# Performance work log

Hardware: AMD Instinct MI355X
Metric: run time of the kernel (lower is better)

## Reference

```python
import jax, jax.numpy as jnp
import numpy as np

TAU_MIN = 0.1
TAU_MAX = 5.0
EPS = 1e-8


def setup_inputs() -> dict:
    key = jax.random.key(0)
    ks = jax.random.split(key, 5)
    B, DK, NK, DV, H = 16384, 512, 4096, 512, 32
    return {
        "q": jax.random.normal(ks[0], (B, DK), dtype=jnp.float32),
        "keys": jax.random.normal(ks[1], (NK, DK), dtype=jnp.float32),
        "values": jax.random.normal(ks[2], (NK, DV), dtype=jnp.float32),
        "w1": jax.random.normal(ks[3], (H, 1), dtype=jnp.float32) * (6.0 / (H + 1)) ** 0.5,
        "b1": jnp.zeros((H,), dtype=jnp.float32),
        "w2": jax.random.normal(ks[4], (1, H), dtype=jnp.float32) * (6.0 / (H + 1)) ** 0.5,
        "b2": jnp.zeros((1,), dtype=jnp.float32),
    }


def reference(q, keys, values, w1, b1, w2, b2):
    d_k = q.shape[-1]
    n_keys = keys.shape[0]
    base_scale = d_k ** -0.5
    max_entropy = np.log(max(n_keys, 2)).astype(np.float32)

    # raw logits: (B, NK)
    raw_logits = jnp.matmul(q, keys.T)

    # entropy of base-scaled softmax
    p = jax.nn.softmax(raw_logits * base_scale, axis=-1)
    entropy = -jnp.sum(p * jnp.log(p + EPS), axis=-1, keepdims=True)  # (B,1)
    entropy = jnp.clip(entropy / (max_entropy + EPS), 0.0, 1.0)

    # entropy -> tau via tiny MLP (exact GELU, matching torch default)
    h = jax.nn.gelu(entropy @ w1.T + b1, approximate=False)  # (B,H)
    scale = jax.nn.sigmoid(h @ w2.T + b2)                    # (B,1)
    tau = TAU_MIN + (TAU_MAX - TAU_MIN) * scale

    # re-scaled softmax and final matmul
    scaled_logits = raw_logits * base_scale / (tau + EPS)
    attn_weights = jax.nn.softmax(scaled_logits, axis=-1)    # (B, NK)
    output = jnp.matmul(attn_weights, values)                # (B, DV)
    return output, attn_weights, entropy, tau
```

## Files before the change

### kernel.cpp

```cpp
#include <hip/hip_runtime.h>
#include <math.h>

#define B_ROWS 16384
#define DK     512
#define NK     4096
#define DV     512
#define H_MLP  32

typedef __attribute__((ext_vector_type(8))) short s16x8;
typedef __attribute__((ext_vector_type(4))) short s16x4;
typedef __attribute__((ext_vector_type(4))) float f32x4;

__device__ __forceinline__ short f2bf(float f) {
  unsigned u = __float_as_uint(f);
  u += 0x7fffu + ((u >> 16) & 1u);
  return (short)(u >> 16);
}

__device__ __forceinline__ void async_cp16(const short* g, short* l) {
  __builtin_amdgcn_global_load_lds(
      (const __attribute__((address_space(1))) unsigned int*)g,
      (__attribute__((address_space(3))) unsigned int*)l, 16, 0, 0);
}

__global__ __launch_bounds__(256) void cvt_bf16(const float* __restrict__ src,
                                                short* __restrict__ dst,
                                                long n, float scale) {
  long i = ((long)blockIdx.x * 256 + threadIdx.x) * 8;
  if (i >= n) return;
  float4 a = *(const float4*)(src + i);
  float4 b = *(const float4*)(src + i + 4);
  s16x8 o;
  o[0] = f2bf(a.x * scale); o[1] = f2bf(a.y * scale);
  o[2] = f2bf(a.z * scale); o[3] = f2bf(a.w * scale);
  o[4] = f2bf(b.x * scale); o[5] = f2bf(b.y * scale);
  o[6] = f2bf(b.z * scale); o[7] = f2bf(b.w * scale);
  *(s16x8*)(dst + i) = o;
}

__global__ __launch_bounds__(256) void transpose_v(const float* __restrict__ v,
                                                   short* __restrict__ vT) {
  __shared__ float tile[32][33];
  const int tx = threadIdx.x & 31;
  const int ty = threadIdx.x >> 5;
  const int k0 = blockIdx.x * 32;
  const int n0 = blockIdx.y * 32;
#pragma unroll
  for (int j = 0; j < 4; ++j)
    tile[ty + j * 8][tx] = v[(long)(k0 + ty + j * 8) * DV + n0 + tx];
  __syncthreads();
#pragma unroll
  for (int j = 0; j < 4; ++j)
    vT[(long)(n0 + ty + j * 8) * NK + k0 + tx] = f2bf(tile[tx][ty + j * 8]);
}

__device__ __forceinline__ void stage_f32_sw(const float* __restrict__ src, int ldk,
                                             int row0, int k0, short* lds, int tid) {
#pragma unroll
  for (int i = 0; i < 4; ++i) {
    int f   = i * 256 + tid;
    int row = f >> 3;
    int p   = f & 7;
    int c   = p ^ (row & 7);
    const float* gp = src + (long)(row0 + row) * ldk + k0 + c * 8;
    float4 a = *(const float4*)gp;
    float4 b = *(const float4*)(gp + 4);
    s16x8 o;
    o[0] = f2bf(a.x); o[1] = f2bf(a.y); o[2] = f2bf(a.z); o[3] = f2bf(a.w);
    o[4] = f2bf(b.x); o[5] = f2bf(b.y); o[6] = f2bf(b.z); o[7] = f2bf(b.w);
    *(s16x8*)(lds + row * 64 + p * 8) = o;
  }
}

template <int RPW>
__device__ __forceinline__ void stage_bf_async(const short* __restrict__ src, int ldk,
                                               int row0, int k0, short* lds,
                                               int w, int lane) {
  const int srow = lane >> 3;
  const int c    = (lane & 7) ^ srow;
  const short* g = src + (long)(row0 + w * RPW + srow) * ldk + k0 + c * 8;
  short* lb = lds + w * RPW * 64;
#pragma unroll
  for (int i = 0; i < RPW / 8; ++i)
    async_cp16(g + (long)(i * 8) * ldk, lb + i * 512);
}

template <int AMODE, int BMODE>
__global__ __launch_bounds__(256) void gemm_nt(const void* __restrict__ Av,
                                               const void* __restrict__ Bv,
                                               float* __restrict__ C,
                                               int M, int N, int K, float alpha) {
  __shared__ short As[128 * 64];
  __shared__ short Bs[128 * 64];
  const int tid = threadIdx.x;

  const int nwg = gridDim.x * gridDim.y;
  const int bid = blockIdx.y * gridDim.x + blockIdx.x;
  const int per = nwg >> 3;
  const int swz = (bid & 7) * per + (bid >> 3);
  const int bx  = swz % gridDim.x;
  const int by  = swz / gridDim.x;

  const int rowBase = by * 128;
  const int colBase = bx * 128;
  const int w = tid >> 6, lane = tid & 63;
  const int waveM = w >> 1, waveN = w & 1;
  const int quad = lane >> 4, lr = lane & 15;
  const int sw = lr & 7;

  f32x4 acc[4][4];
#pragma unroll
  for (int i = 0; i < 4; ++i)
#pragma unroll
    for (int j = 0; j < 4; ++j)
      acc[i][j] = (f32x4){0.f, 0.f, 0.f, 0.f};

  for (int k0 = 0; k0 < K; k0 += 64) {
    __syncthreads();
    if constexpr (AMODE)
      stage_bf_async<32>((const short*)Av, K, rowBase, k0, As, w, lane);
    else
      stage_f32_sw((const float*)Av, K, rowBase, k0, As, tid);
    if constexpr (BMODE)
      stage_bf_async<32>((const short*)Bv, K, colBase, k0, Bs, w, lane);
    else
      stage_f32_sw((const float*)Bv, K, colBase, k0, Bs, tid);
    __syncthreads();
#pragma unroll
    for (int ks = 0; ks < 2; ++ks) {
      const int cpos = ((ks * 4 + quad) ^ sw) * 8;
      s16x8 a[4], b[4];
#pragma unroll
      for (int t = 0; t < 4; ++t) {
        a[t] = *(const s16x8*)(As + (waveM * 64 + t * 16 + lr) * 64 + cpos);
        b[t] = *(const s16x8*)(Bs + (waveN * 64 + t * 16 + lr) * 64 + cpos);
      }
#pragma unroll
      for (int mt = 0; mt < 4; ++mt)
#pragma unroll
        for (int nt = 0; nt < 4; ++nt)
          acc[mt][nt] = __builtin_amdgcn_mfma_f32_16x16x32_bf16(a[mt], b[nt], acc[mt][nt], 0, 0, 0);
    }
  }

#pragma unroll
  for (int mt = 0; mt < 4; ++mt)
#pragma unroll
    for (int nt = 0; nt < 4; ++nt) {
      int col = colBase + waveN * 64 + nt * 16 + lr;
#pragma unroll
      for (int r = 0; r < 4; ++r) {
        int row = rowBase + waveM * 64 + mt * 16 + quad * 4 + r;
        C[(long)row * N + col] = acc[mt][nt][r] * alpha;
      }
    }
}

template <int BM, int BN, int WM, int WN>
__global__ __launch_bounds__(WM * WN * 64, 2) void gemm_nt_2ph(
    const short* __restrict__ A, const short* __restrict__ B,
    float* __restrict__ C, int M, int N, int K, float alpha) {
  constexpr int NWAVE = WM * WN;
  constexpr int MR = BM / WM / 16;
  constexpr int NR = BN / WN / 16;
  __shared__ short As[2 * BM * 64];
  __shared__ short Bs[2 * BN * 64];

  const int tid = threadIdx.x;
  const int nwg = gridDim.x * gridDim.y;
  const int bid = blockIdx.y * gridDim.x + blockIdx.x;
  const int per = nwg >> 3;
  const int swz = (bid & 7) * per + (bid >> 3);
  const int bx  = swz % gridDim.x;
  const int by  = swz / gridDim.x;

  const int rowBase = by * BM;
  const int colBase = bx * BN;
  const int w = tid >> 6, lane = tid & 63;
  const int waveM = w / WN, waveN = w % WN;
  const int quad = lane >> 4, lr = lane & 15, sw = lr & 7;

  f32x4 acc[MR][NR];
#pragma unroll
  for (int i = 0; i < MR; ++i)
#pragma unroll
    for (int j = 0; j < NR; ++j)
      acc[i][j] = (f32x4){0.f, 0.f, 0.f, 0.f};

  auto compute = [&](const short* Ab, const short* Bb) {
#pragma unroll
    for (int ks = 0; ks < 2; ++ks) {
      const int cpos = ((ks * 4 + quad) ^ sw) * 8;
      s16x8 a[MR], b[NR];
#pragma unroll
      for (int mt = 0; mt < MR; ++mt)
        a[mt] = *(const s16x8*)(Ab + (waveM * (BM / WM) + mt * 16 + lr) * 64 + cpos);
#pragma unroll
      for (int nt = 0; nt < NR; ++nt)
        b[nt] = *(const s16x8*)(Bb + (waveN * (BN / WN) + nt * 16 + lr) * 64 + cpos);
      __builtin_amdgcn_s_setprio(1);
#pragma unroll
      for (int mt = 0; mt < MR; ++mt)
#pragma unroll
        for (int nt = 0; nt < NR; ++nt)
          acc[mt][nt] = __builtin_amdgcn_mfma_f32_16x16x32_bf16(a[mt], b[nt], acc[mt][nt], 0, 0, 0);
      __builtin_amdgcn_s_setprio(0);
    }
  };

  const int NT = K >> 6;

  stage_bf_async<BM / NWAVE>(A, K, rowBase, 0, As, w, lane);
  stage_bf_async<BN / NWAVE>(B, K, colBase, 0, Bs, w, lane);
  asm volatile("s_waitcnt vmcnt(0)" ::: "memory");
  __builtin_amdgcn_s_barrier();
  __builtin_amdgcn_sched_barrier(0);

  int cur = 0;
  for (int t = 0; t < NT - 1; ++t) {
    const int nxt = cur ^ 1;
    stage_bf_async<BM / NWAVE>(A, K, rowBase, (t + 1) * 64, As + nxt * BM * 64, w, lane);
    stage_bf_async<BN / NWAVE>(B, K, colBase, (t + 1) * 64, Bs + nxt * BN * 64, w, lane);
    __builtin_amdgcn_sched_barrier(0);
    compute(As + cur * BM * 64, Bs + cur * BN * 64);
    asm volatile("s_waitcnt vmcnt(0)" ::: "memory");
    __builtin_amdgcn_s_barrier();
    __builtin_amdgcn_sched_barrier(0);
    cur = nxt;
  }
  compute(As + cur * BM * 64, Bs + cur * BN * 64);

#pragma unroll
  for (int mt = 0; mt < MR; ++mt)
#pragma unroll
    for (int nt = 0; nt < NR; ++nt) {
      int col = colBase + waveN * (BN / WN) + nt * 16 + lr;
#pragma unroll
      for (int r = 0; r < 4; ++r) {
        int row = rowBase + waveM * (BM / WM) + mt * 16 + quad * 4 + r;
        C[(long)row * N + col] = acc[mt][nt][r] * alpha;
      }
    }
}

__global__ __launch_bounds__(256) void entropy_softmax(
    float* __restrict__ l, short* __restrict__ attn_bf,
    float* __restrict__ ent_out, float* __restrict__ tau_out,
    const float* __restrict__ w1, const float* __restrict__ b1,
    const float* __restrict__ w2, const float* __restrict__ b2) {
  const int wid = threadIdx.x >> 6, lane = threadIdx.x & 63;
  const int row = blockIdx.x * 4 + wid;
  float4* lr = (float4*)(l + (long)row * NK);

  float4 v[16];
#pragma unroll
  for (int it = 0; it < 16; ++it) v[it] = lr[it * 64 + lane];

  float m = -3.4e38f;
#pragma unroll
  for (int it = 0; it < 16; ++it)
    m = fmaxf(m, fmaxf(fmaxf(v[it].x, v[it].y), fmaxf(v[it].z, v[it].w)));
#pragma unroll
  for (int off = 32; off >= 1; off >>= 1) m = fmaxf(m, __shfl_xor(m, off));

  float Z = 0.f, E1 = 0.f;
#pragma unroll
  for (int it = 0; it < 16; ++it) {
    float e0 = __expf(v[it].x - m), e1 = __expf(v[it].y - m);
    float e2 = __expf(v[it].z - m), e3 = __expf(v[it].w - m);
    Z  += (e0 + e1) + (e2 + e3);
    E1 += v[it].x * e0 + v[it].y * e1 + v[it].z * e2 + v[it].w * e3;
  }
#pragma unroll
  for (int off = 32; off >= 1; off >>= 1) {
    Z  += __shfl_xor(Z, off);
    E1 += __shfl_xor(E1, off);
  }

  float entropy = m + __logf(Z) - E1 / Z;
  float en = fminf(fmaxf(entropy / 8.3177662f, 0.f), 1.f);

  float hp = 0.f;
  if (lane < H_MLP) {
    float x = en * w1[lane] + b1[lane];
    float g = 0.5f * x * (1.f + erff(x * 0.70710678f));
    hp = g * w2[lane];
  }
#pragma unroll
  for (int off = 16; off >= 1; off >>= 1) hp += __shfl_xor(hp, off);
  hp = __shfl(hp, 0);

  float s    = 1.f / (1.f + __expf(-(hp + b2[0])));
  float tau  = 0.1f + 4.9f * s;
  float itau = 1.f / (tau + 1e-8f);
  if (lane == 0) { ent_out[row] = en; tau_out[row] = tau; }

  const float mi = m * itau;
  float Z2 = 0.f;
#pragma unroll
  for (int it = 0; it < 16; ++it) {
    v[it].x = __expf(fmaf(v[it].x, itau, -mi));
    v[it].y = __expf(fmaf(v[it].y, itau, -mi));
    v[it].z = __expf(fmaf(v[it].z, itau, -mi));
    v[it].w = __expf(fmaf(v[it].w, itau, -mi));
    Z2 += (v[it].x + v[it].y) + (v[it].z + v[it].w);
  }
#pragma unroll
  for (int off = 32; off >= 1; off >>= 1) Z2 += __shfl_xor(Z2, off);
  const float inv = 1.f / Z2;

  short* br = attn_bf ? attn_bf + (long)row * NK : nullptr;
#pragma unroll
  for (int it = 0; it < 16; ++it) {
    float4 p;
    p.x = v[it].x * inv; p.y = v[it].y * inv;
    p.z = v[it].z * inv; p.w = v[it].w * inv;
    lr[it * 64 + lane] = p;
    if (br) {
      s16x4 o;
      o.x = f2bf(p.x); o.y = f2bf(p.y); o.z = f2bf(p.z); o.w = f2bf(p.w);
      *(s16x4*)(br + (it * 64 + lane) * 4) = o;
    }
  }
}

extern "C" void kernel_launch(void* const* d_in, const int* in_sizes, int n_in,
                              void* d_out, int out_size, void* d_ws, size_t ws_size,
                              hipStream_t stream) {
  const float* q    = (const float*)d_in[0];
  const float* keys = (const float*)d_in[1];
  const float* vals = (const float*)d_in[2];
  const float* w1   = (const float*)d_in[3];
  const float* b1   = (const float*)d_in[4];
  const float* w2   = (const float*)d_in[5];
  const float* b2   = (const float*)d_in[6];

  float* out  = (float*)d_out;
  float* attn = out + (long)B_ROWS * DV;
  float* ent  = attn + (long)B_ROWS * NK;
  float* tau  = ent + B_ROWS;

  char* ws = (char*)d_ws;
  const size_t off_vT    = 0;
  const size_t off_keysb = off_vT + (size_t)DV * NK * 2;
  const size_t off_qb    = off_keysb + (size_t)NK * DK * 2;
  const size_t off_attnb = off_qb + (size_t)B_ROWS * DK * 2;
  const size_t need_mid  = off_attnb;
  const size_t need_full = off_attnb + (size_t)B_ROWS * NK * 2;

  short* vT    = (short*)(ws + off_vT);
  short* keysb = (short*)(ws + off_keysb);
  short* qb    = (short*)(ws + off_qb);
  short* attnb = (short*)(ws + off_attnb);

  const float base_scale = 0.044194173824159216f;

  transpose_v<<<dim3(NK / 32, DV / 32), 256, 0, stream>>>(vals, vT);

  if (ws_size >= need_mid) {
    cvt_bf16<<<(int)(((long)B_ROWS * DK) / 2048), 256, 0, stream>>>(
        q, qb, (long)B_ROWS * DK, base_scale);
    cvt_bf16<<<(int)(((long)NK * DK) / 2048), 256, 0, stream>>>(
        keys, keysb, (long)NK * DK, 1.0f);
    gemm_nt_2ph<256, 256, 2, 4><<<dim3(NK / 256, B_ROWS / 256), 512, 0, stream>>>(
        qb, keysb, attn, B_ROWS, NK, DK, 1.0f);
  } else {
    gemm_nt<0, 0><<<dim3(NK / 128, B_ROWS / 128), 256, 0, stream>>>(
        q, keys, attn, B_ROWS, NK, DK, base_scale);
  }

  const bool full = ws_size >= need_full;
  entropy_softmax<<<B_ROWS / 4, 256, 0, stream>>>(
      attn, full ? attnb : nullptr, ent, tau, w1, b1, w2, b2);

  if (full)
    gemm_nt_2ph<128, 128, 2, 2><<<dim3(DV / 128, B_ROWS / 128), 256, 0, stream>>>(
        attnb, vT, out, B_ROWS, DV, NK, 1.0f);
  else
    gemm_nt<0, 1><<<dim3(DV / 128, B_ROWS / 128), 256, 0, stream>>>(
        attn, vT, out, B_ROWS, DV, NK, 1.0f);
}
```

Before: 609.3 us.

## Replace double-buffered GEMM with 4-stage K=32 async LDS pipeline

Measured after the change: 648.9 us. 1.06x slower.

```diff
diff --git a/kernel.cpp b/kernel.cpp
--- a/kernel.cpp
+++ b/kernel.cpp
@@ -156,15 +156,30 @@
     }
 }
 
+__device__ __forceinline__ void stage32(const short* __restrict__ src, int ldk,
+                                        int row0, int k0, short* lds,
+                                        int w, int lane) {
+  const int r16 = lane >> 2;
+  const int p   = lane & 3;
+  const int c   = p ^ ((r16 & 3) ^ (r16 >> 2));
+  const short* g = src + (long)(row0 + w * 32 + r16) * ldk + k0 + c * 8;
+  short* lb = lds + w * 32 * 32;
+  async_cp16(g, lb);
+  async_cp16(g + (long)16 * ldk, lb + 16 * 32);
+}
+
 template <int BM, int BN, int WM, int WN>
-__global__ __launch_bounds__(WM * WN * 64, 2) void gemm_nt_2ph(
+__global__ __launch_bounds__(WM * WN * 64, 2) void gemm_nt_p4(
     const short* __restrict__ A, const short* __restrict__ B,
     float* __restrict__ C, int M, int N, int K, float alpha) {
   constexpr int NWAVE = WM * WN;
   constexpr int MR = BM / WM / 16;
   constexpr int NR = BN / WN / 16;
-  __shared__ short As[2 * BM * 64];
-  __shared__ short Bs[2 * BN * 64];
+  constexpr int ASZ = BM * 32;
+  constexpr int BSZ = BN * 32;
+  static_assert(BM / NWAVE == 32 && BN / NWAVE == 32, "stage32 geometry");
+  __shared__ short As[4 * ASZ];
+  __shared__ short Bs[4 * BSZ];
 
   const int tid = threadIdx.x;
   const int nwg = gridDim.x * gridDim.y;
@@ -178,7 +193,9 @@
   const int colBase = bx * BN;
   const int w = tid >> 6, lane = tid & 63;
   const int waveM = w / WN, waveN = w % WN;
-  const int quad = lane >> 4, lr = lane & 15, sw = lr & 7;
+  const int quad = lane >> 4, lr = lane & 15;
+  const int sw2 = (lr & 3) ^ (lr >> 2);
+  const int cpos = (quad ^ sw2) * 8;
 
   f32x4 acc[MR][NR];
 #pragma unroll
@@ -188,47 +205,44 @@
       acc[i][j] = (f32x4){0.f, 0.f, 0.f, 0.f};
 
   auto compute = [&](const short* Ab, const short* Bb) {
-#pragma unroll
-    for (int ks = 0; ks < 2; ++ks) {
-      const int cpos = ((ks * 4 + quad) ^ sw) * 8;
-      s16x8 a[MR], b[NR];
-#pragma unroll
-      for (int mt = 0; mt < MR; ++mt)
-        a[mt] = *(const s16x8*)(Ab + (waveM * (BM / WM) + mt * 16 + lr) * 64 + cpos);
+    s16x8 a[MR], b[NR];
+#pragma unroll
+    for (int mt = 0; mt < MR; ++mt)
+      a[mt] = *(const s16x8*)(Ab + (waveM * (BM / WM) + mt * 16 + lr) * 32 + cpos);
+#pragma unroll
+    for (int nt = 0; nt < NR; ++nt)
+      b[nt] = *(const s16x8*)(Bb + (waveN * (BN / WN) + nt * 16 + lr) * 32 + cpos);
+    __builtin_amdgcn_s_setprio(1);
+#pragma unroll
+    for (int mt = 0; mt < MR; ++mt)
 #pragma unroll
       for (int nt = 0; nt < NR; ++nt)
-        b[nt] = *(const s16x8*)(Bb + (waveN * (BN / WN) + nt * 16 + lr) * 64 + cpos);
-      __builtin_amdgcn_s_setprio(1);
-#pragma unroll
-      for (int mt = 0; mt < MR; ++mt)
-#pragma unroll
-        for (int nt = 0; nt < NR; ++nt)
-          acc[mt][nt] = __builtin_amdgcn_mfma_f32_16x16x32_bf16(a[mt], b[nt], acc[mt][nt], 0, 0, 0);
-      __builtin_amdgcn_s_setprio(0);
-    }
+        acc[mt][nt] = __builtin_amdgcn_mfma_f32_16x16x32_bf16(a[mt], b[nt], acc[mt][nt], 0, 0, 0);
+    __builtin_amdgcn_s_setprio(0);
   };
 
-  const int NT = K >> 6;
-
-  stage_bf_async<BM / NWAVE>(A, K, rowBase, 0, As, w, lane);
-  stage_bf_async<BN / NWAVE>(B, K, colBase, 0, Bs, w, lane);
-  asm volatile("s_waitcnt vmcnt(0)" ::: "memory");
-  __builtin_amdgcn_s_barrier();
-  __builtin_amdgcn_sched_barrier(0);
-
-  int cur = 0;
-  for (int t = 0; t < NT - 1; ++t) {
-    const int nxt = cur ^ 1;
-    stage_bf_async<BM / NWAVE>(A, K, rowBase, (t + 1) * 64, As + nxt * BM * 64, w, lane);
-    stage_bf_async<BN / NWAVE>(B, K, colBase, (t + 1) * 64, Bs + nxt * BN * 64, w, lane);
-    __builtin_amdgcn_sched_barrier(0);
-    compute(As + cur * BM * 64, Bs + cur * BN * 64);
-    asm volatile("s_waitcnt vmcnt(0)" ::: "memory");
+  const int NT = K >> 5;
+
+#pragma unroll
+  for (int pt = 0; pt < 3; ++pt) {
+    stage32(A, K, rowBase, pt * 32, As + pt * ASZ, w, lane);
+    stage32(B, K, colBase, pt * 32, Bs + pt * BSZ, w, lane);
+  }
+
+  for (int t = 0; t < NT; ++t) {
+    const int ahead = (t + 2 <= NT - 1) ? 2 : (NT - 1 - t);
+    if (ahead == 2)      asm volatile("s_waitcnt vmcnt(8)" ::: "memory");
+    else if (ahead == 1) asm volatile("s_waitcnt vmcnt(4)" ::: "memory");
+    else                 asm volatile("s_waitcnt vmcnt(0)" ::: "memory");
     __builtin_amdgcn_s_barrier();
     __builtin_amdgcn_sched_barrier(0);
-    cur = nxt;
-  }
-  compute(As + cur * BM * 64, Bs + cur * BN * 64);
+    if (t + 3 < NT) {
+      stage32(A, K, rowBase, (t + 3) * 32, As + ((t + 3) & 3) * ASZ, w, lane);
+      stage32(B, K, colBase, (t + 3) * 32, Bs + ((t + 3) & 3) * BSZ, w, lane);
+    }
+    __builtin_amdgcn_sched_barrier(0);
+    compute(As + (t & 3) * ASZ, Bs + (t & 3) * BSZ);
+  }
 
 #pragma unroll
   for (int mt = 0; mt < MR; ++mt)
@@ -362,7 +376,7 @@
         q, qb, (long)B_ROWS * DK, base_scale);
     cvt_bf16<<<(int)(((long)NK * DK) / 2048), 256, 0, stream>>>(
         keys, keysb, (long)NK * DK, 1.0f);
-    gemm_nt_2ph<256, 256, 2, 4><<<dim3(NK / 256, B_ROWS / 256), 512, 0, stream>>>(
+    gemm_nt_p4<256, 256, 2, 4><<<dim3(NK / 256, B_ROWS / 256), 512, 0, stream>>>(
         qb, keysb, attn, B_ROWS, NK, DK, 1.0f);
   } else {
     gemm_nt<0, 0><<<dim3(NK / 128, B_ROWS / 128), 256, 0, stream>>>(
@@ -374,7 +388,7 @@
       attn, full ? attnb : nullptr, ent, tau, w1, b1, w2, b2);
 
   if (full)
-    gemm_nt_2ph<128, 128, 2, 2><<<dim3(DV / 128, B_ROWS / 128), 256, 0, stream>>>(
+    gemm_nt_p4<128, 128, 2, 2><<<dim3(DV / 128, B_ROWS / 128), 256, 0, stream>>>(
         attnb, vT, out, B_ROWS, DV, NK, 1.0f);
   else
     gemm_nt<0, 1><<<dim3(DV / 128, B_ROWS / 128), 256, 0, stream>>>(
```
